# Optimization experiments

Measured on AMD Instinct MI355X. Metric: run time of the kernel, lower is better.

## Reference

```python
import math
import jax, jax.numpy as jnp
import numpy as np

B, L, D, DK = 2, 2046, 1024, 64
H, GH, LH = 16, 8, 8   # total / global / local heads
WS = 3                  # hardcoded window_size in source
MAX_VAL = 1e9


def setup_inputs() -> dict:
    key = jax.random.key(0)
    ks = jax.random.split(key, 7)
    x = jax.random.normal(ks[0], (B, L, D), dtype=jnp.float32)
    mask = jnp.ones((B, 1, L, L), dtype=jnp.float32)
    s = 0.02
    Wq = jax.random.normal(ks[1], (D, D), dtype=jnp.float32) * s   # torch Linear weight [out,in]
    bq = jnp.zeros((D,), dtype=jnp.float32)
    Wk = jax.random.normal(ks[2], (H, DK, DK), dtype=jnp.float32) * s
    bk = jnp.zeros((H, DK), dtype=jnp.float32)
    Wv = jax.random.normal(ks[3], (H, DK, DK), dtype=jnp.float32) * s
    bv = jnp.zeros((H, DK), dtype=jnp.float32)
    return {"x": x, "mask": mask, "Wq": Wq, "bq": bq,
            "Wk": Wk, "bk": bk, "Wv": Wv, "bv": bv}


def reference(x, mask, Wq, bq, Wk, bk, Wv, bv):
    b, l, d = x.shape
    scale = 1.0 / math.sqrt(DK)

    q = x @ Wq.T + bq                                   # [b,l,d]
    q = q.reshape(b, l, H, DK).transpose(0, 2, 1, 3)    # [b,h,l,dk]
    kv = x.reshape(b, l, H, DK).transpose(0, 2, 1, 3)   # k and v are both raw x

    # ---------------- global heads: full attention ----------------
    qg = q[:, :GH]                                      # [b,gh,l,dk]
    kg = kv[:, :GH]
    kgp = jnp.einsum('bhli,hoi->bhlo', kg, Wk[:GH]) + bk[:GH][None, :, None, :]
    vgp = jnp.einsum('bhli,hoi->bhlo', kg, Wv[:GH]) + bv[:GH][None, :, None, :]
    sg = jnp.einsum('bhld,bhmd->bhlm', qg, kgp) * scale  # [b,gh,l,l]
    mfull = (mask[:, 0] == 0)[:, None]                   # [b,1,l,l]
    sg = jnp.where(mfull, -MAX_VAL, sg)
    pg = jax.nn.softmax(sg, axis=-1)
    vg = jnp.einsum('bhlm,bhmd->bhld', pg, vgp)          # [b,gh,l,dk]

    # ---------------- local heads: window-pooled attention ----------------
    nw = l // WS
    ql = q[:, GH:]                                       # [b,lh,l,dk]
    kl = kv[:, GH:]
    # mean-pool keys over non-overlapping windows (pool_method='mean');
    # source uses the SAME pooled tensor for both K and V (repeat(2,...))
    kw = kl.reshape(b, LH, nw, WS, DK).mean(axis=3)      # [b,lh,nw,dk]
    # window mask: majority of window columns valid, per query row
    wm = mask[:, 0].reshape(b, l, nw, WS).sum(-1) >= math.ceil(WS / 2)  # [b,l,nw]
    klp = jnp.einsum('bhni,hoi->bhno', kw, Wk[GH:]) + bk[GH:][None, :, None, :]
    vlp = jnp.einsum('bhni,hoi->bhno', kw, Wv[GH:]) + bv[GH:][None, :, None, :]
    sl = jnp.einsum('bhld,bhnd->bhln', ql, klp) * scale  # [b,lh,l,nw]
    sl = jnp.where(~wm[:, None], -MAX_VAL, sl)
    pl = jax.nn.softmax(sl, axis=-1)
    vl = jnp.einsum('bhln,bhnd->bhld', pl, vlp)          # [b,lh,l,dk]

    value_all = jnp.concatenate([vg, vl], axis=1)        # [b,h,l,dk]
    return (value_all, pg, pl)
```

## Files before the change

kernel.cpp:

```cpp
#include <hip/hip_runtime.h>
#include <hip/hip_bf16.h>
#include <stdint.h>

typedef __bf16 bf16;
typedef bf16 bf16x8 __attribute__((ext_vector_type(8)));
typedef float f32x4 __attribute__((ext_vector_type(4)));

#define B_ 2
#define L_ 2046
#define H_ 16
#define NW_ 682
#define LP_ 2048
#define NWP_ 704
#define M_ (B_*L_)
#define SCALE_ 0.125f
#define VTP 280

__device__ inline bf16x8 zf8() {
  bf16x8 v;
#pragma unroll
  for (int e = 0; e < 8; ++e) v[e] = (bf16)0.0f;
  return v;
}

__device__ inline uint32_t pkbf(float a, float b) {
  uint16_t ua = __builtin_bit_cast(uint16_t, (bf16)a);
  uint16_t ub = __builtin_bit_cast(uint16_t, (bf16)b);
  return (uint32_t)ua | ((uint32_t)ub << 16);
}
__device__ inline float upk_lo(uint32_t u) { return __builtin_bit_cast(float, u << 16); }
__device__ inline float upk_hi(uint32_t u) { return __builtin_bit_cast(float, u & 0xffff0000u); }

__global__ __launch_bounds__(256) void cast4(const float* __restrict__ in,
                                             bf16* __restrict__ out, int n) {
  int i = (blockIdx.x * 256 + threadIdx.x) * 4;
  if (i + 3 < n) {
    float4 v = *reinterpret_cast<const float4*>(in + i);
    bf16 tmp[4];
    tmp[0] = (bf16)v.x; tmp[1] = (bf16)v.y; tmp[2] = (bf16)v.z; tmp[3] = (bf16)v.w;
    *reinterpret_cast<uint64_t*>(out + i) = *reinterpret_cast<const uint64_t*>(tmp);
  } else {
    for (; i < n; ++i) out[i] = (bf16)in[i];
  }
}

__global__ __launch_bounds__(256) void qgemm_t(const bf16* __restrict__ X,
                                               const bf16* __restrict__ W,
                                               const float* __restrict__ bq,
                                               bf16* __restrict__ Q) {
  __shared__ bf16 As[64 * 40];
  __shared__ bf16 Bs[128 * 40];
  int t = threadIdx.x, lane = t & 63, w = t >> 6;
  int lid = lane & 15, g = lane >> 4;
  int m0 = blockIdx.x * 64, n0 = blockIdx.y * 128;
  int wm = (w >> 1) * 32, wn = (w & 1) * 64;
  f32x4 z4 = {0.f, 0.f, 0.f, 0.f};
  f32x4 acc[2][4];
#pragma unroll
  for (int mi = 0; mi < 2; ++mi)
#pragma unroll
    for (int ni = 0; ni < 4; ++ni) acc[mi][ni] = z4;
  int r1 = t >> 2, c1 = t & 3;
  for (int k0 = 0; k0 < 1024; k0 += 32) {
    int ga = m0 + r1; if (ga >= M_) ga = M_ - 1;
    bf16x8 av = *reinterpret_cast<const bf16x8*>(X + (size_t)ga * 1024 + k0 + c1 * 8);
    bf16x8 bv1 = *reinterpret_cast<const bf16x8*>(W + (size_t)(n0 + r1) * 1024 + k0 + c1 * 8);
    bf16x8 bv2 = *reinterpret_cast<const bf16x8*>(W + (size_t)(n0 + 64 + r1) * 1024 + k0 + c1 * 8);
    __syncthreads();
    *reinterpret_cast<bf16x8*>(As + r1 * 40 + c1 * 8) = av;
    *reinterpret_cast<bf16x8*>(Bs + r1 * 40 + c1 * 8) = bv1;
    *reinterpret_cast<bf16x8*>(Bs + (64 + r1) * 40 + c1 * 8) = bv2;
    __syncthreads();
    bf16x8 af[2], bfr[4];
#pragma unroll
    for (int mi = 0; mi < 2; ++mi)
      af[mi] = *reinterpret_cast<const bf16x8*>(As + (wm + mi * 16 + lid) * 40 + g * 8);
#pragma unroll
    for (int ni = 0; ni < 4; ++ni)
      bfr[ni] = *reinterpret_cast<const bf16x8*>(Bs + (wn + ni * 16 + lid) * 40 + g * 8);
#pragma unroll
    for (int mi = 0; mi < 2; ++mi)
#pragma unroll
      for (int ni = 0; ni < 4; ++ni)
        acc[mi][ni] = __builtin_amdgcn_mfma_f32_16x16x32_bf16(af[mi], bfr[ni], acc[mi][ni], 0, 0, 0);
  }
  float bias[4];
#pragma unroll
  for (int ni = 0; ni < 4; ++ni) bias[ni] = bq[n0 + wn + ni * 16 + lid];
#pragma unroll
  for (int mi = 0; mi < 2; ++mi)
#pragma unroll
    for (int r = 0; r < 4; ++r) {
      int row = m0 + wm + mi * 16 + g * 4 + r;
      if (row < M_) {
#pragma unroll
        for (int ni = 0; ni < 4; ++ni)
          Q[(size_t)row * 1024 + n0 + wn + ni * 16 + lid] = (bf16)(acc[mi][ni][r] + bias[ni]);
      }
    }
}

__global__ __launch_bounds__(256) void proj_g32(const float* __restrict__ x,
    const float* __restrict__ Wk, const float* __restrict__ bk,
    const float* __restrict__ Wv, const float* __restrict__ bv,
    bf16* __restrict__ KGP, bf16* __restrict__ VGP) {
  __shared__ float xs[64][64];
  __shared__ float wks[64][65];
  __shared__ float wvs[64][65];
  int t = threadIdx.x;
  int lb = blockIdx.x, bh = blockIdx.y;
  int b = bh >> 3, h = bh & 7;
  int l0 = lb * 64;
  for (int idx = t; idx < 4096; idx += 256) {
    int r = idx >> 6, c = idx & 63;
    int l = l0 + r;
    xs[r][c] = (l < L_) ? x[((size_t)b * L_ + l) * 1024 + h * 64 + c] : 0.0f;
    wks[r][c] = Wk[(size_t)h * 4096 + idx];
    wvs[r][c] = Wv[(size_t)h * 4096 + idx];
  }
  __syncthreads();
  int o = t & 63, lg = t >> 6;
  float kbias = bk[h * 64 + o], vbias = bv[h * 64 + o];
  const size_t outb = (size_t)bh * LP_ * 64;
  for (int ls = 0; ls < 16; ++ls) {
    int l = lg * 16 + ls;
    float ka = kbias, va = vbias;
#pragma unroll
    for (int i = 0; i < 64; ++i) {
      float xv = xs[l][i];
      ka = fmaf(xv, wks[o][i], ka);
      va = fmaf(xv, wvs[o][i], va);
    }
    KGP[outb + (size_t)(l0 + l) * 64 + o] = (bf16)ka;
    VGP[outb + (size_t)(l0 + l) * 64 + o] = (bf16)va;
  }
}

__global__ __launch_bounds__(256) void proj_l32(const float* __restrict__ x,
    const float* __restrict__ Wk, const float* __restrict__ bk,
    const float* __restrict__ Wv, const float* __restrict__ bv,
    bf16* __restrict__ KLP, bf16* __restrict__ VLP) {
  __shared__ float xs[64][64];
  __shared__ float wks[64][65];
  __shared__ float wvs[64][65];
  int t = threadIdx.x;
  int nb = blockIdx.x, bh = blockIdx.y;
  int b = bh >> 3, h = bh & 7;
  int n0 = nb * 64;
  int hh = 8 + h;
  for (int idx = t; idx < 4096; idx += 256) {
    int r = idx >> 6, c = idx & 63;
    int n = n0 + r;
    float v = 0.0f;
    if (n < NW_) {
      size_t base = ((size_t)b * L_ + 3 * n) * 1024 + hh * 64 + c;
      v = (x[base] + x[base + 1024] + x[base + 2048]) * (1.0f / 3.0f);
    }
    xs[r][c] = v;
    wks[r][c] = Wk[(size_t)hh * 4096 + idx];
    wvs[r][c] = Wv[(size_t)hh * 4096 + idx];
  }
  __syncthreads();
  int o = t & 63, lg = t >> 6;
  float kbias = bk[hh * 64 + o], vbias = bv[hh * 64 + o];
  const size_t outb = (size_t)bh * NWP_ * 64;
  for (int ls = 0; ls < 16; ++ls) {
    int l = lg * 16 + ls;
    float ka = kbias, va = vbias;
#pragma unroll
    for (int i = 0; i < 64; ++i) {
      float xv = xs[l][i];
      ka = fmaf(xv, wks[o][i], ka);
      va = fmaf(xv, wvs[o][i], va);
    }
    KLP[outb + (size_t)(n0 + l) * 64 + o] = (bf16)ka;
    VLP[outb + (size_t)(n0 + l) * 64 + o] = (bf16)va;
  }
}

__global__ __launch_bounds__(256) void maskprep(const float* __restrict__ mask,
                                                uint64_t* __restrict__ gm,
                                                uint64_t* __restrict__ wm) {
  int row = blockIdx.x * 4 + (threadIdx.x >> 6);
  int lane = threadIdx.x & 63;
  if (row >= B_ * L_) return;
  int b = row / L_, l = row % L_;
  const float* mr = mask + (size_t)b * L_ * L_ + (size_t)l * L_;
  for (int w = 0; w < 32; ++w) {
    int m = w * 64 + lane;
    bool masked = (m >= L_) ? true : (mr[m] == 0.0f);
    uint64_t bal = __ballot(masked);
    if (lane == 0) gm[(size_t)row * 32 + w] = bal;
  }
  for (int w = 0; w < 11; ++w) {
    int n = w * 64 + lane;
    bool lmask = true;
    if (n < NW_) {
      float s = mr[3 * n] + mr[3 * n + 1] + mr[3 * n + 2];
      lmask = !(s >= 2.0f);
    }
    uint64_t bal = __ballot(lmask);
    if (lane == 0) wm[(size_t)row * 11 + w] = bal;
  }
}

__global__ __launch_bounds__(512, 2) void attn_gf(const bf16* __restrict__ Q,
    const bf16* __restrict__ K, const bf16* __restrict__ V,
    const uint64_t* __restrict__ GM,
    float* __restrict__ OP, float* __restrict__ OV) {
  __shared__ float sums[128];
  __shared__ float strip[16][257];
  __shared__ bf16 vt[64][VTP];
  int t = threadIdx.x;
  int lane = t & 63, wave = t >> 6;
  int lid = lane & 15, g = lane >> 4;
  int q0 = blockIdx.x * 16;
  int bh = blockIdx.y;
  int b = bh >> 3, h = bh & 7;
  const bf16* qb = Q + (size_t)b * L_ * 1024 + h * 64;
  const bf16* kb = K + (size_t)bh * LP_ * 64;
  const bf16* vpb = V + (size_t)bh * LP_ * 64;
  const uint64_t* gmb = GM + (size_t)b * L_ * 32;

  bf16x8 aq0 = zf8(), aq1 = zf8();
  {
    int qr = q0 + lid;
    if (qr < L_) {
      aq0 = *reinterpret_cast<const bf16x8*>(qb + (size_t)qr * 1024 + g * 8);
      aq1 = *reinterpret_cast<const bf16x8*>(qb + (size_t)qr * 1024 + 32 + g * 8);
    }
  }
  uint32_t preg[32];
  float rs[4] = {0.f, 0.f, 0.f, 0.f};
#pragma unroll
  for (int it = 0; it < 8; ++it) {
    int p = it * 8 + wave;
    int c0 = p * 32;
    int col0 = c0 + lid, col1 = c0 + 16 + lid;
    bf16x8 bka0 = *reinterpret_cast<const bf16x8*>(kb + (size_t)col0 * 64 + g * 8);
    bf16x8 bka1 = *reinterpret_cast<const bf16x8*>(kb + (size_t)col0 * 64 + 32 + g * 8);
    bf16x8 bkb0 = *reinterpret_cast<const bf16x8*>(kb + (size_t)col1 * 64 + g * 8);
    bf16x8 bkb1 = *reinterpret_cast<const bf16x8*>(kb + (size_t)col1 * 64 + 32 + g * 8);
    f32x4 acc0 = {0.f, 0.f, 0.f, 0.f}, acc1 = {0.f, 0.f, 0.f, 0.f};
    acc0 = __builtin_amdgcn_mfma_f32_16x16x32_bf16(aq0, bka0, acc0, 0, 0, 0);
    acc0 = __builtin_amdgcn_mfma_f32_16x16x32_bf16(aq1, bka1, acc0, 0, 0, 0);
    acc1 = __builtin_amdgcn_mfma_f32_16x16x32_bf16(aq0, bkb0, acc1, 0, 0, 0);
    acc1 = __builtin_amdgcn_mfma_f32_16x16x32_bf16(aq1, bkb1, acc1, 0, 0, 0);
    int wi = c0 >> 6;
    int bit0 = c0 & 32;
#pragma unroll
    for (int r = 0; r < 4; ++r) {
      int qr = q0 + g * 4 + r;
      uint64_t w = (qr < L_) ? gmb[(size_t)qr * 32 + wi] : ~0ull;
      float pv0 = ((w >> (bit0 + lid)) & 1) ? 0.0f : __expf(acc0[r] * SCALE_);
      float pv1 = ((w >> (bit0 + 16 + lid)) & 1) ? 0.0f : __expf(acc1[r] * SCALE_);
      rs[r] += pv0 + pv1;
      preg[it * 4 + r] = pkbf(pv0, pv1);
    }
  }
#pragma unroll
  for (int off = 8; off >= 1; off >>= 1)
#pragma unroll
    for (int r = 0; r < 4; ++r) rs[r] += __shfl_xor(rs[r], off, 64);
  if (lid == 0) {
#pragma unroll
    for (int r = 0; r < 4; ++r) sums[wave * 16 + g * 4 + r] = rs[r];
  }
  __syncthreads();
  float invr[4];
#pragma unroll
  for (int r = 0; r < 4; ++r) {
    int row = g * 4 + r;
    float s = 0.f;
#pragma unroll
    for (int ww = 0; ww < 8; ++ww) s += sums[ww * 16 + row];
    invr[r] = (s > 0.f) ? 1.0f / s : 0.0f;
  }
  int orow = t >> 5;
  int qrT = q0 + orow;
  bool rowok = (qrT < L_);
  const size_t rowb = (size_t)bh * L_ * L_ + (size_t)(rowok ? qrT : 0) * L_;
  int c8 = (t & 31) * 8;
  int sd = t & 63, mq = t >> 6;
  f32x4 vacc[4];
  f32x4 z4 = {0.f, 0.f, 0.f, 0.f};
#pragma unroll
  for (int dg = 0; dg < 4; ++dg) vacc[dg] = z4;
#pragma unroll
  for (int it = 0; it < 8; ++it) {
    int mb0 = it * 256;
#pragma unroll
    for (int r = 0; r < 4; ++r) {
      uint32_t u = preg[it * 4 + r];
      strip[g * 4 + r][wave * 32 + lid] = upk_lo(u) * invr[r];
      strip[g * 4 + r][wave * 32 + 16 + lid] = upk_hi(u) * invr[r];
    }
#pragma unroll
    for (int blk = 0; blk < 4; ++blk) {
      bf16 st[8];
#pragma unroll
      for (int e = 0; e < 8; ++e)
        st[e] = vpb[(size_t)(mb0 + blk * 64 + mq * 8 + e) * 64 + sd];
      *reinterpret_cast<bf16x8*>(&vt[sd][blk * 64 + mq * 8]) = *reinterpret_cast<const bf16x8*>(st);
    }
    __syncthreads();
    int col = mb0 + c8;
    if (rowok) {
#pragma unroll
      for (int pr = 0; pr < 4; ++pr) {
        int cc = c8 + pr * 2;
        if (col + pr * 2 + 1 < L_) {
          float2 o2 = make_float2(strip[orow][cc], strip[orow][cc + 1]);
          *reinterpret_cast<float2*>(OP + rowb + col + pr * 2) = o2;
        }
      }
    }
    bf16x8 af;
#pragma unroll
    for (int e = 0; e < 8; ++e) af[e] = (bf16)strip[lid][wave * 32 + g * 8 + e];
#pragma unroll
    for (int dg = 0; dg < 4; ++dg) {
      bf16x8 bv8 = *reinterpret_cast<const bf16x8*>(&vt[dg * 16 + lid][wave * 32 + g * 8]);
      vacc[dg] = __builtin_amdgcn_mfma_f32_16x16x32_bf16(af, bv8, vacc[dg], 0, 0, 0);
    }
    __syncthreads();
  }
#pragma unroll
  for (int wsel = 0; wsel < 8; ++wsel) {
    if (wave == wsel) {
#pragma unroll
      for (int dg = 0; dg < 4; ++dg)
#pragma unroll
        for (int r = 0; r < 4; ++r) {
          if (wsel == 0) strip[g * 4 + r][dg * 16 + lid] = vacc[dg][r];
          else           strip[g * 4 + r][dg * 16 + lid] += vacc[dg][r];
        }
    }
    __syncthreads();
  }
  float* ob = OV + (((size_t)b * 16 + h) * L_) * 64;
  for (int idx = t; idx < 1024; idx += 512) {
    int r = idx >> 6, d = idx & 63;
    int qr = q0 + r;
    if (qr < L_) ob[(size_t)qr * 64 + d] = strip[r][d];
  }
}

__global__ __launch_bounds__(512, 2) void attn_lf(const bf16* __restrict__ Q,
    const bf16* __restrict__ K, const bf16* __restrict__ V,
    const uint64_t* __restrict__ WM,
    float* __restrict__ OP, float* __restrict__ OV) {
  __shared__ float sums[128];
  __shared__ float strip[16][257];
  __shared__ bf16 vt[64][VTP];
  int t = threadIdx.x;
  int lane = t & 63, wave = t >> 6;
  int lid = lane & 15, g = lane >> 4;
  int q0 = blockIdx.x * 16;
  int bh = blockIdx.y;
  int b = bh >> 3, h = bh & 7;
  const bf16* qb = Q + (size_t)b * L_ * 1024 + (8 + h) * 64;
  const bf16* kb = K + (size_t)bh * NWP_ * 64;
  const bf16* vpb = V + (size_t)bh * NWP_ * 64;
  const uint64_t* wmb = WM + (size_t)b * L_ * 11;

  bf16x8 aq0 = zf8(), aq1 = zf8();
  {
    int qr = q0 + lid;
    if (qr < L_) {
      aq0 = *reinterpret_cast<const bf16x8*>(qb + (size_t)qr * 1024 + g * 8);
      aq1 = *reinterpret_cast<const bf16x8*>(qb + (size_t)qr * 1024 + 32 + g * 8);
    }
  }
  uint32_t preg[12];
  float rs[4] = {0.f, 0.f, 0.f, 0.f};
#pragma unroll
  for (int it = 0; it < 3; ++it) {
    int p = it * 8 + wave;
    if (p < 22) {
      int c0 = p * 32;
      int col0 = c0 + lid, col1 = c0 + 16 + lid;
      bf16x8 bka0 = *reinterpret_cast<const bf16x8*>(kb + (size_t)col0 * 64 + g * 8);
      bf16x8 bka1 = *reinterpret_cast<const bf16x8*>(kb + (size_t)col0 * 64 + 32 + g * 8);
      bf16x8 bkb0 = *reinterpret_cast<const bf16x8*>(kb + (size_t)col1 * 64 + g * 8);
      bf16x8 bkb1 = *reinterpret_cast<const bf16x8*>(kb + (size_t)col1 * 64 + 32 + g * 8);
      f32x4 acc0 = {0.f, 0.f, 0.f, 0.f}, acc1 = {0.f, 0.f, 0.f, 0.f};
      acc0 = __builtin_amdgcn_mfma_f32_16x16x32_bf16(aq0, bka0, acc0, 0, 0, 0);
      acc0 = __builtin_amdgcn_mfma_f32_16x16x32_bf16(aq1, bka1, acc0, 0, 0, 0);
      acc1 = __builtin_amdgcn_mfma_f32_16x16x32_bf16(aq0, bkb0, acc1, 0, 0, 0);
      acc1 = __builtin_amdgcn_mfma_f32_16x16x32_bf16(aq1, bkb1, acc1, 0, 0, 0);
      int wi = c0 >> 6;
      int bit0 = c0 & 32;
#pragma unroll
      for (int r = 0; r < 4; ++r) {
        int qr = q0 + g * 4 + r;
        uint64_t w = (qr < L_) ? wmb[(size_t)qr * 11 + wi] : ~0ull;
        float pv0 = ((w >> (bit0 + lid)) & 1) ? 0.0f : __expf(acc0[r] * SCALE_);
        float pv1 = ((w >> (bit0 + 16 + lid)) & 1) ? 0.0f : __expf(acc1[r] * SCALE_);
        rs[r] += pv0 + pv1;
        preg[it * 4 + r] = pkbf(pv0, pv1);
      }
    }
  }
#pragma unroll
  for (int off = 8; off >= 1; off >>= 1)
#pragma unroll
    for (int r = 0; r < 4; ++r) rs[r] += __shfl_xor(rs[r], off, 64);
  if (lid == 0) {
#pragma unroll
    for (int r = 0; r < 4; ++r) sums[wave * 16 + g * 4 + r] = rs[r];
  }
  __syncthreads();
  float invr[4];
#pragma unroll
  for (int r = 0; r < 4; ++r) {
    int row = g * 4 + r;
    float s = 0.f;
#pragma unroll
    for (int ww = 0; ww < 8; ++ww) s += sums[ww * 16 + row];
    invr[r] = (s > 0.f) ? 1.0f / s : 0.0f;
  }
  int orow = t >> 5;
  int qrT = q0 + orow;
  bool rowok = (qrT < L_);
  const size_t rowb = (size_t)bh * L_ * NW_ + (size_t)(rowok ? qrT : 0) * NW_;
  int c8 = (t & 31) * 8;
  int sd = t & 63, mq = t >> 6;
  f32x4 vacc[4];
  f32x4 z4 = {0.f, 0.f, 0.f, 0.f};
#pragma unroll
  for (int dg = 0; dg < 4; ++dg) vacc[dg] = z4;
#pragma unroll
  for (int it = 0; it < 3; ++it) {
    int p = it * 8 + wave;
    bool act = (p < 22);
    int mb0 = it * 256;
    if (act) {
#pragma unroll
      for (int r = 0; r < 4; ++r) {
        uint32_t u = preg[it * 4 + r];
        strip[g * 4 + r][wave * 32 + lid] = upk_lo(u) * invr[r];
        strip[g * 4 + r][wave * 32 + 16 + lid] = upk_hi(u) * invr[r];
      }
    }
#pragma unroll
    for (int blk = 0; blk < 4; ++blk) {
      bf16 st[8];
#pragma unroll
      for (int e = 0; e < 8; ++e) {
        int m = mb0 + blk * 64 + mq * 8 + e;
        if (m >= NWP_) m = NWP_ - 1;
        st[e] = vpb[(size_t)m * 64 + sd];
      }
      *reinterpret_cast<bf16x8*>(&vt[sd][blk * 64 + mq * 8]) = *reinterpret_cast<const bf16x8*>(st);
    }
    __syncthreads();
    int col = mb0 + c8;
    if (rowok) {
#pragma unroll
      for (int pr = 0; pr < 4; ++pr) {
        int cc = c8 + pr * 2;
        if (col + pr * 2 + 1 < NW_) {
          float2 o2 = make_float2(strip[orow][cc], strip[orow][cc + 1]);
          *reinterpret_cast<float2*>(OP + rowb + col + pr * 2) = o2;
        }
      }
    }
    if (act) {
      bf16x8 af;
#pragma unroll
      for (int e = 0; e < 8; ++e) af[e] = (bf16)strip[lid][wave * 32 + g * 8 + e];
#pragma unroll
      for (int dg = 0; dg < 4; ++dg) {
        bf16x8 bv8 = *reinterpret_cast<const bf16x8*>(&vt[dg * 16 + lid][wave * 32 + g * 8]);
        vacc[dg] = __builtin_amdgcn_mfma_f32_16x16x32_bf16(af, bv8, vacc[dg], 0, 0, 0);
      }
    }
    __syncthreads();
  }
#pragma unroll
  for (int wsel = 0; wsel < 8; ++wsel) {
    if (wave == wsel) {
#pragma unroll
      for (int dg = 0; dg < 4; ++dg)
#pragma unroll
        for (int r = 0; r < 4; ++r) {
          if (wsel == 0) strip[g * 4 + r][dg * 16 + lid] = vacc[dg][r];
          else           strip[g * 4 + r][dg * 16 + lid] += vacc[dg][r];
        }
    }
    __syncthreads();
  }
  float* ob = OV + (((size_t)b * 16 + 8 + h) * L_) * 64;
  for (int idx = t; idx < 1024; idx += 512) {
    int r = idx >> 6, d = idx & 63;
    int qr = q0 + r;
    if (qr < L_) ob[(size_t)qr * 64 + d] = strip[r][d];
  }
}

extern "C" void kernel_launch(void* const* d_in, const int* in_sizes, int n_in,
                              void* d_out, int out_size, void* d_ws, size_t ws_size,
                              hipStream_t stream) {
  (void)in_sizes; (void)n_in; (void)out_size; (void)ws_size;
  const float* x    = (const float*)d_in[0];
  const float* mask = (const float*)d_in[1];
  const float* Wq   = (const float*)d_in[2];
  const float* bq   = (const float*)d_in[3];
  const float* Wk   = (const float*)d_in[4];
  const float* bk   = (const float*)d_in[5];
  const float* Wv   = (const float*)d_in[6];
  const float* bv   = (const float*)d_in[7];

  char* ws = (char*)d_ws;
  bf16* qbb     = (bf16*)(ws + 0);
  bf16* kgb     = (bf16*)(ws + 8380416);
  bf16* vgb     = (bf16*)(ws + 12574720);
  bf16* klb     = (bf16*)(ws + 16769024);
  bf16* vlb     = (bf16*)(ws + 18210816);
  uint64_t* gm  = (uint64_t*)(ws + 19652608);
  uint64_t* wm  = (uint64_t*)(ws + 20700160);
  bf16* xbb     = (bf16*)(ws + 21060256);
  bf16* wqb     = (bf16*)(ws + 29440672);

  float* out    = (float*)d_out;
  float* o_vall = out;
  float* o_pg   = out + 4190208;
  float* o_pl   = out + 71168064;

  cast4<<<4092, 256, 0, stream>>>(x, xbb, 4190208);
  cast4<<<1024, 256, 0, stream>>>(Wq, wqb, 1048576);
  qgemm_t<<<dim3(64, 8), 256, 0, stream>>>(xbb, wqb, bq, qbb);
  proj_g32<<<dim3(32, 16), 256, 0, stream>>>(x, Wk, bk, Wv, bv, kgb, vgb);
  proj_l32<<<dim3(11, 16), 256, 0, stream>>>(x, Wk, bk, Wv, bv, klb, vlb);
  maskprep<<<1023, 256, 0, stream>>>(mask, gm, wm);

  attn_gf<<<dim3(128, 16), 512, 0, stream>>>(qbb, kgb, vgb, gm, o_pg, o_vall);
  attn_lf<<<dim3(128, 16), 512, 0, stream>>>(qbb, klb, vlb, wm, o_pl, o_vall);
}
```

Baseline: 407.5 us.

## Store V projections transposed and read MFMA B operand directly from global

```diff
diff --git a/kernel.cpp b/kernel.cpp
--- a/kernel.cpp
+++ b/kernel.cpp
@@ -14,7 +14,6 @@
 #define NWP_ 704
 #define M_ (B_*L_)
 #define SCALE_ 0.125f
-#define VTP 280
 
 __device__ inline bf16x8 zf8() {
   bf16x8 v;
@@ -103,7 +102,7 @@
 __global__ __launch_bounds__(256) void proj_g32(const float* __restrict__ x,
     const float* __restrict__ Wk, const float* __restrict__ bk,
     const float* __restrict__ Wv, const float* __restrict__ bv,
-    bf16* __restrict__ KGP, bf16* __restrict__ VGP) {
+    bf16* __restrict__ KGP, bf16* __restrict__ VGT) {
   __shared__ float xs[64][64];
   __shared__ float wks[64][65];
   __shared__ float wvs[64][65];
@@ -121,6 +120,7 @@
   __syncthreads();
   int o = t & 63, lg = t >> 6;
   float kbias = bk[h * 64 + o], vbias = bv[h * 64 + o];
+  float vacc[16];
   const size_t outb = (size_t)bh * LP_ * 64;
   for (int ls = 0; ls < 16; ++ls) {
     int l = lg * 16 + ls;
@@ -132,14 +132,22 @@
       va = fmaf(xv, wvs[o][i], va);
     }
     KGP[outb + (size_t)(l0 + l) * 64 + o] = (bf16)ka;
-    VGP[outb + (size_t)(l0 + l) * 64 + o] = (bf16)va;
+    vacc[ls] = va;
+  }
+  __syncthreads();
+#pragma unroll
+  for (int ls = 0; ls < 16; ++ls) wvs[o][lg * 16 + ls] = vacc[ls];
+  __syncthreads();
+  for (int idx = t; idx < 4096; idx += 256) {
+    int oo = idx >> 6, ll = idx & 63;
+    VGT[(size_t)bh * 64 * LP_ + (size_t)oo * LP_ + l0 + ll] = (bf16)wvs[oo][ll];
   }
 }
 
 __global__ __launch_bounds__(256) void proj_l32(const float* __restrict__ x,
     const float* __restrict__ Wk, const float* __restrict__ bk,
     const float* __restrict__ Wv, const float* __restrict__ bv,
-    bf16* __restrict__ KLP, bf16* __restrict__ VLP) {
+    bf16* __restrict__ KLP, bf16* __restrict__ VLT) {
   __shared__ float xs[64][64];
   __shared__ float wks[64][65];
   __shared__ float wvs[64][65];
@@ -163,6 +171,7 @@
   __syncthreads();
   int o = t & 63, lg = t >> 6;
   float kbias = bk[hh * 64 + o], vbias = bv[hh * 64 + o];
+  float vacc[16];
   const size_t outb = (size_t)bh * NWP_ * 64;
   for (int ls = 0; ls < 16; ++ls) {
     int l = lg * 16 + ls;
@@ -174,7 +183,15 @@
       va = fmaf(xv, wvs[o][i], va);
     }
     KLP[outb + (size_t)(n0 + l) * 64 + o] = (bf16)ka;
-    VLP[outb + (size_t)(n0 + l) * 64 + o] = (bf16)va;
+    vacc[ls] = va;
+  }
+  __syncthreads();
+#pragma unroll
+  for (int ls = 0; ls < 16; ++ls) wvs[o][lg * 16 + ls] = vacc[ls];
+  __syncthreads();
+  for (int idx = t; idx < 4096; idx += 256) {
+    int oo = idx >> 6, ll = idx & 63;
+    VLT[(size_t)bh * 64 * NWP_ + (size_t)oo * NWP_ + n0 + ll] = (bf16)wvs[oo][ll];
   }
 }
 
@@ -205,12 +222,11 @@
 }
 
 __global__ __launch_bounds__(512, 2) void attn_gf(const bf16* __restrict__ Q,
-    const bf16* __restrict__ K, const bf16* __restrict__ V,
+    const bf16* __restrict__ K, const bf16* __restrict__ VT,
     const uint64_t* __restrict__ GM,
     float* __restrict__ OP, float* __restrict__ OV) {
   __shared__ float sums[128];
-  __shared__ float strip[16][257];
-  __shared__ bf16 vt[64][VTP];
+  __shared__ float strip2[2][16][257];
   int t = threadIdx.x;
   int lane = t & 63, wave = t >> 6;
   int lid = lane & 15, g = lane >> 4;
@@ -219,7 +235,7 @@
   int b = bh >> 3, h = bh & 7;
   const bf16* qb = Q + (size_t)b * L_ * 1024 + h * 64;
   const bf16* kb = K + (size_t)bh * LP_ * 64;
-  const bf16* vpb = V + (size_t)bh * LP_ * 64;
+  const bf16* vtg = VT + (size_t)bh * 64 * LP_;
   const uint64_t* gmb = GM + (size_t)b * L_ * 32;
 
   bf16x8 aq0 = zf8(), aq1 = zf8();
@@ -281,27 +297,19 @@
   bool rowok = (qrT < L_);
   const size_t rowb = (size_t)bh * L_ * L_ + (size_t)(rowok ? qrT : 0) * L_;
   int c8 = (t & 31) * 8;
-  int sd = t & 63, mq = t >> 6;
   f32x4 vacc[4];
   f32x4 z4 = {0.f, 0.f, 0.f, 0.f};
 #pragma unroll
   for (int dg = 0; dg < 4; ++dg) vacc[dg] = z4;
 #pragma unroll
   for (int it = 0; it < 8; ++it) {
+    float* sbuf = &strip2[it & 1][0][0];
     int mb0 = it * 256;
 #pragma unroll
     for (int r = 0; r < 4; ++r) {
       uint32_t u = preg[it * 4 + r];
-      strip[g * 4 + r][wave * 32 + lid] = upk_lo(u) * invr[r];
-      strip[g * 4 + r][wave * 32 + 16 + lid] = upk_hi(u) * invr[r];
-    }
-#pragma unroll
-    for (int blk = 0; blk < 4; ++blk) {
-      bf16 st[8];
-#pragma unroll
-      for (int e = 0; e < 8; ++e)
-        st[e] = vpb[(size_t)(mb0 + blk * 64 + mq * 8 + e) * 64 + sd];
-      *reinterpret_cast<bf16x8*>(&vt[sd][blk * 64 + mq * 8]) = *reinterpret_cast<const bf16x8*>(st);
+      sbuf[(g * 4 + r) * 257 + wave * 32 + lid] = upk_lo(u) * invr[r];
+      sbuf[(g * 4 + r) * 257 + wave * 32 + 16 + lid] = upk_hi(u) * invr[r];
     }
     __syncthreads();
     int col = mb0 + c8;
@@ -310,21 +318,22 @@
       for (int pr = 0; pr < 4; ++pr) {
         int cc = c8 + pr * 2;
         if (col + pr * 2 + 1 < L_) {
-          float2 o2 = make_float2(strip[orow][cc], strip[orow][cc + 1]);
+          float2 o2 = make_float2(sbuf[orow * 257 + cc], sbuf[orow * 257 + cc + 1]);
           *reinterpret_cast<float2*>(OP + rowb + col + pr * 2) = o2;
         }
       }
     }
     bf16x8 af;
 #pragma unroll
-    for (int e = 0; e < 8; ++e) af[e] = (bf16)strip[lid][wave * 32 + g * 8 + e];
+    for (int e = 0; e < 8; ++e) af[e] = (bf16)sbuf[lid * 257 + wave * 32 + g * 8 + e];
 #pragma unroll
     for (int dg = 0; dg < 4; ++dg) {
-      bf16x8 bv8 = *reinterpret_cast<const bf16x8*>(&vt[dg * 16 + lid][wave * 32 + g * 8]);
+      bf16x8 bv8 = *reinterpret_cast<const bf16x8*>(vtg + (size_t)(dg * 16 + lid) * LP_ + mb0 + wave * 32 + g * 8);
       vacc[dg] = __builtin_amdgcn_mfma_f32_16x16x32_bf16(af, bv8, vacc[dg], 0, 0, 0);
     }
-    __syncthreads();
-  }
+  }
+  __syncthreads();
+  float* red = &strip2[0][0][0];
 #pragma unroll
   for (int wsel = 0; wsel < 8; ++wsel) {
     if (wave == wsel) {
@@ -332,8 +341,8 @@
       for (int dg = 0; dg < 4; ++dg)
 #pragma unroll
         for (int r = 0; r < 4; ++r) {
-          if (wsel == 0) strip[g * 4 + r][dg * 16 + lid] = vacc[dg][r];
-          else           strip[g * 4 + r][dg * 16 + lid] += vacc[dg][r];
+          if (wsel == 0) red[(g * 4 + r) * 257 + dg * 16 + lid] = vacc[dg][r];
+          else           red[(g * 4 + r) * 257 + dg * 16 + lid] += vacc[dg][r];
         }
     }
     __syncthreads();
@@ -342,17 +351,16 @@
   for (int idx = t; idx < 1024; idx += 512) {
     int r = idx >> 6, d = idx & 63;
     int qr = q0 + r;
-    if (qr < L_) ob[(size_t)qr * 64 + d] = strip[r][d];
+    if (qr < L_) ob[(size_t)qr * 64 + d] = red[r * 257 + d];
   }
 }
 
 __global__ __launch_bounds__(512, 2) void attn_lf(const bf16* __restrict__ Q,
-    const bf16* __restrict__ K, const bf16* __restrict__ V,
+    const bf16* __restrict__ K, const bf16* __restrict__ VT,
     const uint64_t* __restrict__ WM,
     float* __restrict__ OP, float* __restrict__ OV) {
   __shared__ float sums[128];
-  __shared__ float strip[16][257];
-  __shared__ bf16 vt[64][VTP];
+  __shared__ float strip2[2][16][257];
   int t = threadIdx.x;
   int lane = t & 63, wave = t >> 6;
   int lid = lane & 15, g = lane >> 4;
@@ -361,7 +369,7 @@
   int b = bh >> 3, h = bh & 7;
   const bf16* qb = Q + (size_t)b * L_ * 1024 + (8 + h) * 64;
   const bf16* kb = K + (size_t)bh * NWP_ * 64;
-  const bf16* vpb = V + (size_t)bh * NWP_ * 64;
+  const bf16* vtg = VT + (size_t)bh * 64 * NWP_;
   const uint64_t* wmb = WM + (size_t)b * L_ * 11;
 
   bf16x8 aq0 = zf8(), aq1 = zf8();
@@ -425,13 +433,13 @@
   bool rowok = (qrT < L_);
   const size_t rowb = (size_t)bh * L_ * NW_ + (size_t)(rowok ? qrT : 0) * NW_;
   int c8 = (t & 31) * 8;
-  int sd = t & 63, mq = t >> 6;
   f32x4 vacc[4];
   f32x4 z4 = {0.f, 0.f, 0.f, 0.f};
 #pragma unroll
   for (int dg = 0; dg < 4; ++dg) vacc[dg] = z4;
 #pragma unroll
   for (int it = 0; it < 3; ++it) {
+    float* sbuf = &strip2[it & 1][0][0];
     int p = it * 8 + wave;
     bool act = (p < 22);
     int mb0 = it * 256;
@@ -439,20 +447,9 @@
 #pragma unroll
       for (int r = 0; r < 4; ++r) {
         uint32_t u = preg[it * 4 + r];
-        strip[g * 4 + r][wave * 32 + lid] = upk_lo(u) * invr[r];
-        strip[g * 4 + r][wave * 32 + 16 + lid] = upk_hi(u) * invr[r];
+        sbuf[(g * 4 + r) * 257 + wave * 32 + lid] = upk_lo(u) * invr[r];
+        sbuf[(g * 4 + r) * 257 + wave * 32 + 16 + lid] = upk_hi(u) * invr[r];
       }
-    }
-#pragma unroll
-    for (int blk = 0; blk < 4; ++blk) {
-      bf16 st[8];
-#pragma unroll
-      for (int e = 0; e < 8; ++e) {
-        int m = mb0 + blk * 64 + mq * 8 + e;
-        if (m >= NWP_) m = NWP_ - 1;
-        st[e] = vpb[(size_t)m * 64 + sd];
-      }
-      *reinterpret_cast<bf16x8*>(&vt[sd][blk * 64 + mq * 8]) = *reinterpret_cast<const bf16x8*>(st);
     }
     __syncthreads();
     int col = mb0 + c8;
@@ -461,7 +458,7 @@
       for (int pr = 0; pr < 4; ++pr) {
         int cc = c8 + pr * 2;
         if (col + pr * 2 + 1 < NW_) {
-          float2 o2 = make_float2(strip[orow][cc], strip[orow][cc + 1]);
+          float2 o2 = make_float2(sbuf[orow * 257 + cc], sbuf[orow * 257 + cc + 1]);
           *reinterpret_cast<float2*>(OP + rowb + col + pr * 2) = o2;
         }
       }
@@ -469,15 +466,16 @@
     if (act) {
       bf16x8 af;
 #pragma unroll
-      for (int e = 0; e < 8; ++e) af[e] = (bf16)strip[lid][wave * 32 + g * 8 + e];
+      for (int e = 0; e < 8; ++e) af[e] = (bf16)sbuf[lid * 257 + wave * 32 + g * 8 + e];
 #pragma unroll
       for (int dg = 0; dg < 4; ++dg) {
-        bf16x8 bv8 = *reinterpret_cast<const bf16x8*>(&vt[dg * 16 + lid][wave * 32 + g * 8]);
+        bf16x8 bv8 = *reinterpret_cast<const bf16x8*>(vtg + (size_t)(dg * 16 + lid) * NWP_ + mb0 + wave * 32 + g * 8);
         vacc[dg] = __builtin_amdgcn_mfma_f32_16x16x32_bf16(af, bv8, vacc[dg], 0, 0, 0);
       }
     }
-    __syncthreads();
-  }
+  }
+  __syncthreads();
+  float* red = &strip2[0][0][0];
 #pragma unroll
   for (int wsel = 0; wsel < 8; ++wsel) {
     if (wave == wsel) {
@@ -485,8 +483,8 @@
       for (int dg = 0; dg < 4; ++dg)
 #pragma unroll
         for (int r = 0; r < 4; ++r) {
-          if (wsel == 0) strip[g * 4 + r][dg * 16 + lid] = vacc[dg][r];
-          else           strip[g * 4 + r][dg * 16 + lid] += vacc[dg][r];
+          if (wsel == 0) red[(g * 4 + r) * 257 + dg * 16 + lid] = vacc[dg][r];
+          else           red[(g * 4 + r) * 257 + dg * 16 + lid] += vacc[dg][r];
         }
     }
     __syncthreads();
@@ -495,7 +493,7 @@
   for (int idx = t; idx < 1024; idx += 512) {
     int r = idx >> 6, d = idx & 63;
     int qr = q0 + r;
-    if (qr < L_) ob[(size_t)qr * 64 + d] = strip[r][d];
+    if (qr < L_) ob[(size_t)qr * 64 + d] = red[r * 257 + d];
   }
 }
 
@@ -515,9 +513,9 @@
   char* ws = (char*)d_ws;
   bf16* qbb     = (bf16*)(ws + 0);
   bf16* kgb     = (bf16*)(ws + 8380416);
-  bf16* vgb     = (bf16*)(ws + 12574720);
+  bf16* vgT     = (bf16*)(ws + 12574720);
   bf16* klb     = (bf16*)(ws + 16769024);
-  bf16* vlb     = (bf16*)(ws + 18210816);
+  bf16* vlT     = (bf16*)(ws + 18210816);
   uint64_t* gm  = (uint64_t*)(ws + 19652608);
   uint64_t* wm  = (uint64_t*)(ws + 20700160);
   bf16* xbb     = (bf16*)(ws + 21060256);
@@ -531,10 +529,10 @@
   cast4<<<4092, 256, 0, stream>>>(x, xbb, 4190208);
   cast4<<<1024, 256, 0, stream>>>(Wq, wqb, 1048576);
   qgemm_t<<<dim3(64, 8), 256, 0, stream>>>(xbb, wqb, bq, qbb);
-  proj_g32<<<dim3(32, 16), 256, 0, stream>>>(x, Wk, bk, Wv, bv, kgb, vgb);
-  proj_l32<<<dim3(11, 16), 256, 0, stream>>>(x, Wk, bk, Wv, bv, klb, vlb);
+  proj_g32<<<dim3(32, 16), 256, 0, stream>>>(x, Wk, bk, Wv, bv, kgb, vgT);
+  proj_l32<<<dim3(11, 16), 256, 0, stream>>>(x, Wk, bk, Wv, bv, klb, vlT);
   maskprep<<<1023, 256, 0, stream>>>(mask, gm, wm);
 
-  attn_gf<<<dim3(128, 16), 512, 0, stream>>>(qbb, kgb, vgb, gm, o_pg, o_vall);
-  attn_lf<<<dim3(128, 16), 512, 0, stream>>>(qbb, klb, vlb, wm, o_pl, o_vall);
-}
+  attn_gf<<<dim3(128, 16), 512, 0, stream>>>(qbb, kgb, vgT, gm, o_pg, o_vall);
+  attn_lf<<<dim3(128, 16), 512, 0, stream>>>(qbb, klb, vlT, wm, o_pl, o_vall);
+}
```

Result: faster. 392.9 us (-3.6%).
